# Kernel tuning notes

Hardware: AMD Instinct MI355X
Metric: run time of the kernel (lower is better)

The kernel has to match this reference:

```python
import jax, jax.numpy as jnp
import numpy as np

WS = 8  # window_size

def conv2d(x, w, b, padding=0, dilation=1, groups=1):
    out = jax.lax.conv_general_dilated(
        x, w, window_strides=(1, 1),
        padding=[(padding, padding), (padding, padding)],
        rhs_dilation=(dilation, dilation),
        feature_group_count=groups)
    return out + b[None, :, None, None]

def lrelu(x):
    return jnp.where(x >= 0, x, 0.1 * x)

def ln_cf(x, w, b, eps=1e-6):
    # LayerNorm, channels_first: normalize over channel dim per pixel
    u = x.mean(1, keepdims=True)
    s = ((x - u) ** 2).mean(1, keepdims=True)
    x = (x - u) / jnp.sqrt(s + eps)
    return w[None, :, None, None] * x + b[None, :, None, None]

def window_part(x, ws):
    # b c (h dh) (w dw) -> b (h w) (dh dw c)
    b, c, H, W = x.shape
    h, w = H // ws, W // ws
    x = x.reshape(b, c, h, ws, w, ws).transpose(0, 2, 4, 3, 5, 1)
    return x.reshape(b, h * w, ws * ws * c)

def window_rev(x, ws, H, W, c):
    # b (h w) (dh dw c) -> b c (h dh) (w dw)
    b = x.shape[0]
    h, w = H // ws, W // ws
    x = x.reshape(b, h, w, ws, ws, c).transpose(0, 5, 1, 3, 2, 4)
    return x.reshape(b, c, H, W)

def setup_inputs() -> dict:
    key = jax.random.key(0)
    B, C, H, W = 4, 64, 256, 256
    ws = WS
    E = ws * ws * C  # 4096
    ks = iter(jax.random.split(key, 40))
    def rn(shape, scale=1.0):
        return jax.random.normal(next(ks), shape, jnp.float32) * scale
    z = lambda *s: jnp.zeros(s, jnp.float32)
    d = {}
    d['x'] = rn((B, C, H, W))
    d['Wv'] = rn((C, C, 1, 1), C ** -0.5); d['bv'] = z(C)
    d['Wri'] = rn((C // 4, C, 1, 1), C ** -0.5); d['bri'] = z(C // 4)
    d['Wrc'] = rn((C // 4, C, 1, 1), C ** -0.5); d['brc'] = z(C // 4)
    d['ln_w'] = jnp.ones((C // 4,), jnp.float32); d['ln_b'] = z(C // 4)
    d['Wca'] = rn((C, C // 4, 1, 1), (C // 4) ** -0.5); d['bca'] = z(C)
    d['Wsa'] = rn((1, C // 4, 3, 3), (9 * C // 4) ** -0.5); d['bsa'] = z(1)
    d['Wm1'] = rn((E // 2, E), E ** -0.5); d['bm1'] = z(E // 2)
    d['Wm2'] = rn((E, E // 2), (E // 2) ** -0.5); d['bm2'] = z(E)
    d['Wq'] = rn((C, C), C ** -0.5); d['bq'] = z(C)
    d['Wk'] = rn((C, C), C ** -0.5); d['bk'] = z(C)
    d['Wd1'] = rn((C, 1, 3, 3), 1.0 / 3.0); d['bd1'] = z(C)
    d['Wd2'] = rn((C, 1, 3, 3), 1.0 / 3.0); d['bd2'] = z(C)
    d['Wo'] = rn((C, C, 1, 1), C ** -0.5); d['bo'] = z(C)
    return d

def reference(x, Wv, bv, Wri, bri, Wrc, brc, ln_w, ln_b, Wca, bca, Wsa, bsa,
              Wm1, bm1, Wm2, bm2, Wq, bq, Wk, bk, Wd1, bd1, Wd2, bd2, Wo, bo):
    B, C, H, W = x.shape
    ws = WS
    E = ws * ws * C
    v = conv2d(x, Wv, bv)
    # ---- MaskPre (route) ----
    x1 = lrelu(conv2d(v, Wri, bri))                       # [B,C/4,H,W]
    x_ = lrelu(ln_cf(conv2d(v, Wrc, brc), ln_w, ln_b))    # [B,C/4,H,W]
    ca = jax.nn.sigmoid(conv2d(x_.mean((2, 3), keepdims=True), Wca, bca))  # [B,C,1,1]
    sa = jax.nn.sigmoid(conv2d(x_, Wsa, bsa, padding=1))                   # [B,1,H,W]
    xm = window_part(x1.mean(1, keepdims=True), ws)       # [B,N,ws^2]
    var_x = jnp.var(xm, axis=-1, ddof=1)                  # torch.var is unbiased
    N = var_x.shape[1]
    k_top = N // 2
    _, idx = jax.lax.top_k(-var_x, k_top)                 # k smallest-variance windows
    mask_bin = jnp.ones((B, N), x.dtype).at[jnp.arange(B)[:, None], idx].set(0.0)
    m = jnp.broadcast_to(mask_bin[:, :, None], (B, N, E))
    m = lrelu(m @ Wm1.T + bm1)
    mask = m @ Wm2.T + bm2                                # [B,N,E]
    # ---- windowed attention / skip split ----
    vs = v * sa
    vw = window_part(v, ws)                               # [B,N,ws^2*C]
    vsw = window_part(vs, ws)
    qkw = window_part(jnp.concatenate([x, x], axis=1), ws)  # [B,N,ws^2*2C]
    v1 = vw * mask
    v2 = vsw * (1.0 - mask)
    mask_qk = jnp.concatenate(
        [mask.reshape(B, N, ws * ws, C)] * 2, axis=-1).reshape(B, N, ws * ws * 2 * C)
    qk1 = (qkw * mask_qk).reshape(B, N * ws * ws, 2 * C)
    q1 = (qk1[..., :C] @ Wq.T + bq).reshape(B * N, ws * ws, C)
    k1 = (qk1[..., C:] @ Wk.T + bk).reshape(B * N, ws * ws, C)
    v1r = v1.reshape(B * N, ws * ws, C)
    attn = jax.nn.softmax(q1 @ jnp.swapaxes(k1, -1, -2), axis=-1)  # [BN,ws^2,ws^2]
    f_attn = (attn @ v1r).reshape(B, N, ws * ws * C)
    attn_out = f_attn + v2
    out = window_rev(attn_out, ws, H, W, C)               # [B,C,H,W]
    # ---- spatial conv branch + projections ----
    c1 = conv2d(out, Wd1, bd1, padding=1, groups=C)
    c2 = conv2d(c1, Wd2, bd2, padding=2, dilation=2, groups=C)
    out = jax.nn.gelu(c2, approximate=False) * ca + out
    out = conv2d(out, Wo, bo)
    return out
```

## Files before the change

kernel.cpp:

```cpp
#include <hip/hip_runtime.h>
#include <hip/hip_bf16.h>
#include <math.h>

typedef __attribute__((ext_vector_type(8))) short short8;
typedef __attribute__((ext_vector_type(16))) float f32x16;

__device__ __forceinline__ float lrelu(float x){ return x >= 0.f ? x : 0.1f*x; }
__device__ __forceinline__ float sigmoidf(float x){ return 1.f/(1.f+expf(-x)); }
__device__ __forceinline__ short f2bf(float f){
  __hip_bfloat16 hb = __float2bfloat16(f);
  return *reinterpret_cast<short*>(&hb);
}
__device__ __forceinline__ float bf16f(short s){
  return __uint_as_float(((unsigned)(unsigned short)s)<<16);
}

#define WF(w,part,mt,kt) ((((w)*8 + (part)*4 + (mt)*... 0)
#undef WF
__device__ __forceinline__ int WFofs(int w,int part,int mt,int kt){
  return (((w*2+part)*2+mt)*4+kt)*512;
}

__global__ void k0_combine(const float* __restrict__ Wv, const float* __restrict__ bv,
                           const float* __restrict__ Wri, const float* __restrict__ bri,
                           const float* __restrict__ Wrc, const float* __restrict__ brc,
                           float* __restrict__ WriE, float* __restrict__ briE,
                           float* __restrict__ WrcE, float* __restrict__ brcE){
  int idx = blockIdx.x*256 + threadIdx.x;
  if (idx < 1024){
    int j = idx>>6, c = idx&63;
    float s1=0.f, s2=0.f;
    for (int k=0;k<64;k++){ s1 = fmaf(Wri[j*64+k], Wv[k*64+c], s1); s2 = fmaf(Wrc[j*64+k], Wv[k*64+c], s2); }
    WriE[idx]=s1; WrcE[idx]=s2;
  }
  if (idx < 16){
    float s1=bri[idx], s2=brc[idx];
    for (int k=0;k<64;k++){ s1 = fmaf(Wri[idx*64+k], bv[k], s1); s2 = fmaf(Wrc[idx*64+k], bv[k], s2); }
    briE[idx]=s1; brcE[idx]=s2;
  }
}

__global__ void k_prep(const float* __restrict__ Wq, const float* __restrict__ Wk,
                       const float* __restrict__ Wo, const float* __restrict__ Wv,
                       const float* __restrict__ WriE, const float* __restrict__ WrcE,
                       float* __restrict__ WT, short* __restrict__ WFrag){
  int idx = blockIdx.x*256 + threadIdx.x;
  if (idx < 4096){
    int oc = idx>>6, c = idx&63;
    WT[c*96 + oc] = Wv[idx];
  } else if (idx < 6144){
    int t = idx - 4096;
    int j = (t>>6) & 15, c = t & 63;
    if (t < 1024) WT[c*96 + 64 + j] = WriE[j*64+c];
    else          WT[c*96 + 80 + j] = WrcE[j*64+c];
  }
  if (idx < 3072){
    int w = idx>>10, rem = idx&1023;
    int part = rem>>9, mt = (rem>>8)&1, kt = (rem>>6)&3, lane = rem&63;
    const float* W = (w==0)?Wq:((w==1)?Wk:Wo);
    int j = (mt<<5)|(lane&31);
    int hh = lane>>5;
    short8 frag;
    #pragma unroll
    for (int i=0;i<8;i++){
      int kl = (hh<<2) + (i&3) + ((i>>2)<<3);
      float val = W[j*64 + (kt<<4) + kl];
      short hi = f2bf(val);
      frag[i] = part ? f2bf(val - bf16f(hi)) : hi;
    }
    *(short8*)&WFrag[WFofs(w,part,mt,kt) + (lane<<3)] = frag;
  }
}

__global__ void k_premask1(const float* __restrict__ Wm1, const float* __restrict__ bm1,
                           float* __restrict__ mrow1, float* __restrict__ mrow0){
  __shared__ float red[256];
  int j = blockIdx.x, tid = threadIdx.x;
  const float* row = Wm1 + (size_t)j*4096;
  float s=0.f;
  for (int e=tid;e<4096;e+=256) s += row[e];
  red[tid]=s; __syncthreads();
  for (int o=128;o;o>>=1){ if (tid<o) red[tid]+=red[tid+o]; __syncthreads(); }
  if (tid==0){
    float t = red[0]+bm1[j];
    mrow1[j] = lrelu(t);
    mrow0[j] = lrelu(bm1[j]);
  }
}

__global__ void k_premask2(const float* __restrict__ Wm2, const float* __restrict__ bm2,
                           const float* __restrict__ mrow1, const float* __restrict__ mrow0,
                           float* __restrict__ mask1, float* __restrict__ mask0,
                           float* __restrict__ mask1T, float* __restrict__ mask0T){
  __shared__ float r1[256], r0[256];
  int e = blockIdx.x, tid = threadIdx.x;
  const float* row = Wm2 + (size_t)e*2048;
  float s1=0.f, s0=0.f;
  for (int j=tid;j<2048;j+=256){ float wv=row[j]; s1 = fmaf(wv, mrow1[j], s1); s0 = fmaf(wv, mrow0[j], s0); }
  r1[tid]=s1; r0[tid]=s0; __syncthreads();
  for (int o=128;o;o>>=1){ if (tid<o){ r1[tid]+=r1[tid+o]; r0[tid]+=r0[tid+o]; } __syncthreads(); }
  if (tid==0){
    float m1 = r1[0]+bm2[e], m0 = r0[0]+bm2[e];
    mask1[e]=m1; mask0[e]=m0;
    int p = e>>6, c = e&63;
    mask1T[(c<<6)|p]=m1; mask0T[(c<<6)|p]=m0;
  }
}

__global__ __launch_bounds__(256) void k1_pw(
    const float* __restrict__ x, const float* __restrict__ WT,
    const float* __restrict__ bv,
    const float* __restrict__ briE, const float* __restrict__ brcE,
    const float* __restrict__ ln_w, const float* __restrict__ ln_b,
    float* __restrict__ v, float* __restrict__ x_, float* __restrict__ xm,
    float* __restrict__ bsum){
  __shared__ float wred[4][16];
  int tid = threadIdx.x;
  int b = blockIdx.x >> 8;
  int hw = ((blockIdx.x & 255) << 8) | tid;
  const float* xb = x + (((size_t)b)<<22) + hw;
  float acc[64], r1[16], rc[16];
  #pragma unroll
  for (int oc=0;oc<64;oc++) acc[oc]=0.f;
  #pragma unroll
  for (int j=0;j<16;j++){ r1[j]=0.f; rc[j]=0.f; }
  for (int c=0;c<64;c++){
    float xv = xb[((size_t)c)<<16];
    const float* wrow = WT + c*96;
    #pragma unroll
    for (int oc=0;oc<64;oc++) acc[oc] = fmaf(wrow[oc], xv, acc[oc]);
    #pragma unroll
    for (int j=0;j<16;j++){ r1[j] = fmaf(wrow[64+j], xv, r1[j]); rc[j] = fmaf(wrow[80+j], xv, rc[j]); }
  }
  float* vb = v + (((size_t)b)<<22) + hw;
  #pragma unroll
  for (int oc=0;oc<64;oc++) vb[((size_t)oc)<<16] = acc[oc] + bv[oc];
  float s1=0.f;
  #pragma unroll
  for (int j=0;j<16;j++){ float t = r1[j]+briE[j]; s1 += lrelu(t); }
  xm[(((size_t)b)<<16)+hw] = s1*(1.f/16.f);
  float u=0.f;
  #pragma unroll
  for (int j=0;j<16;j++){ rc[j] += brcE[j]; u += rc[j]; }
  u *= (1.f/16.f);
  float s2=0.f;
  #pragma unroll
  for (int j=0;j<16;j++){ float d = rc[j]-u; s2 += d*d; }
  float inv = 1.0f / sqrtf(s2*(1.f/16.f) + 1e-6f);
  float xs[16];
  #pragma unroll
  for (int j=0;j<16;j++){
    float t = (rc[j]-u)*inv*ln_w[j] + ln_b[j];
    t = lrelu(t);
    xs[j]=t;
    x_[(((size_t)(b*16+j))<<16)+hw] = t;
  }
  int lane = tid & 63, wv_ = tid >> 6;
  #pragma unroll
  for (int j=0;j<16;j++){
    float val = xs[j];
    for (int o=32;o;o>>=1) val += __shfl_down(val, o, 64);
    if (lane==0) wred[wv_][j]=val;
  }
  __syncthreads();
  if (tid<16) bsum[blockIdx.x*16+tid] = wred[0][tid]+wred[1][tid]+wred[2][tid]+wred[3][tid];
}

__global__ __launch_bounds__(256) void k2_sa(const float* __restrict__ x_,
    const float* __restrict__ Wsa, const float* __restrict__ bsa, float* __restrict__ sa){
  int idx = blockIdx.x*256 + threadIdx.x;
  int b = idx>>16; int hw = idx & 65535; int h = hw>>8, wcol = hw & 255;
  float acc = bsa[0];
  for (int ch=0; ch<16; ++ch){
    const float* plane = x_ + (((size_t)(b*16+ch))<<16);
    #pragma unroll
    for (int ky=0;ky<3;ky++){
      int y = h + ky - 1;
      if ((unsigned)y >= 256u) continue;
      #pragma unroll
      for (int kx=0;kx<3;kx++){
        int xx = wcol + kx - 1;
        if ((unsigned)xx >= 256u) continue;
        acc = fmaf(Wsa[ch*9+ky*3+kx], plane[(y<<8)+xx], acc);
      }
    }
  }
  sa[idx] = sigmoidf(acc);
}

__global__ void k3_ca(const float* __restrict__ bsum, const float* __restrict__ Wca,
                      const float* __restrict__ bca, float* __restrict__ ca){
  __shared__ float meanx[4][16];
  int tid = threadIdx.x;
  if (tid < 64){
    int b = tid>>4, j = tid&15;
    float s=0.f;
    for (int blk=0;blk<256;blk++) s += bsum[(b*256+blk)*16 + j];
    meanx[b][j] = s*(1.f/65536.f);
  }
  __syncthreads();
  int b = tid>>6, oc = tid&63;
  float a = bca[oc];
  #pragma unroll
  for (int j=0;j<16;j++) a = fmaf(Wca[oc*16+j], meanx[b][j], a);
  ca[tid] = sigmoidf(a);
}

__global__ void k4a_var(const float* __restrict__ xm, float* __restrict__ var){
  int t = blockIdx.x*256 + threadIdx.x;
  int b = t>>10, n = t&1023, wh = n>>5, ww = n&31;
  const float* base = xm + (((size_t)b)<<16) + (wh<<11) + (ww<<3);
  float s=0.f;
  #pragma unroll
  for (int dh=0;dh<8;dh++){
    #pragma unroll
    for (int dw=0;dw<8;dw++) s += base[(dh<<8)+dw];
  }
  float mean = s*(1.f/64.f);
  float ss=0.f;
  #pragma unroll
  for (int dh=0;dh<8;dh++){
    #pragma unroll
    for (int dw=0;dw<8;dw++){ float d = base[(dh<<8)+dw]-mean; ss += d*d; }
  }
  var[t] = ss*(1.f/63.f);
}

__global__ __launch_bounds__(1024) void k4b_sel(const float* __restrict__ var, float* __restrict__ sel){
  __shared__ float vs[1024];
  int b = blockIdx.x, tid = threadIdx.x;
  float mine = var[b*1024+tid];
  vs[tid]=mine; __syncthreads();
  int rank=0;
  for (int j=0;j<1024;j++){
    float o = vs[j];
    rank += (o < mine) || (o == mine && j < tid);
  }
  sel[b*1024+tid] = (rank >= 512) ? 1.f : 0.f;
}

__global__ __launch_bounds__(256, 3) void k6_attn(
    const float* __restrict__ x, const float* __restrict__ v, const float* __restrict__ sa,
    const float* __restrict__ sel,
    const float* __restrict__ mask1, const float* __restrict__ mask0,
    const float* __restrict__ mask1T, const float* __restrict__ mask0T,
    const short* __restrict__ WFrag,
    const float* __restrict__ bq, const float* __restrict__ bk,
    float* __restrict__ out){
  __shared__ short8 KAlds[2][2][8][64];
  int tid = threadIdx.x;
  int lane = tid & 63, wvi = tid >> 6;
  int wi = wvi >> 1, ht = wvi & 1;
  int l31 = lane & 31, h = lane >> 5;
  int bid = blockIdx.x;
  int blk = ((bid & 7) << 8) | (bid >> 3);
  int wg = (blk << 1) | wi;
  int b = wg >> 10, n = wg & 1023;
  int pix0 = ((n >> 5) << 11) | ((n & 31) << 3);
  bool sel1 = sel[wg] > 0.5f;
  const float* mrow  = sel1 ? mask1  : mask0;
  const float* mrowT = sel1 ? mask1T : mask0T;
  size_t cbase = (((size_t)b) << 22) + pix0;

  int p = (ht<<5) | l31;
  int po = ((p>>3)<<8) | (p&7);
  size_t gp = cbase + po;
  const float* mr = mrow + (p<<6);
  short8 XBh[4], XBl[4];
  #pragma unroll
  for (int kt=0;kt<4;kt++){
    float4 ma = *(const float4*)&mr[(kt<<4)+(h<<2)];
    float4 mb = *(const float4*)&mr[(kt<<4)+(h<<2)+8];
    float xv[8];
    #pragma unroll
    for (int i=0;i<8;i++){
      int c = (kt<<4) + (h<<2) + (i&3) + ((i>>2)<<3);
      xv[i] = x[gp + ((size_t)c<<16)];
    }
    xv[0]*=ma.x; xv[1]*=ma.y; xv[2]*=ma.z; xv[3]*=ma.w;
    xv[4]*=mb.x; xv[5]*=mb.y; xv[6]*=mb.z; xv[7]*=mb.w;
    short8 fh, fl;
    #pragma unroll
    for (int i=0;i<8;i++){
      short hi = f2bf(xv[i]); fh[i]=hi; fl[i]=f2bf(xv[i]-bf16f(hi));
    }
    XBh[kt]=fh; XBl[kt]=fl;
  }

  short8 QBh[4], QBl[4];
  #pragma unroll
  for (int mt=0;mt<2;mt++){
    f32x16 acc;
    #pragma unroll
    for (int r=0;r<16;r++) acc[r]=0.f;
    #pragma unroll
    for (int kt=0;kt<4;kt++){
      short8 WAh = *(const short8*)&WFrag[WFofs(0,0,mt,kt) + (lane<<3)];
      short8 WAl = *(const short8*)&WFrag[WFofs(0,1,mt,kt) + (lane<<3)];
      acc = __builtin_amdgcn_mfma_f32_32x32x16_bf16(WAh, XBh[kt], acc, 0,0,0);
      acc = __builtin_amdgcn_mfma_f32_32x32x16_bf16(WAh, XBl[kt], acc, 0,0,0);
      acc = __builtin_amdgcn_mfma_f32_32x32x16_bf16(WAl, XBh[kt], acc, 0,0,0);
    }
    #pragma unroll
    for (int rr=0;rr<4;rr++){
      float4 b4 = *(const float4*)&bq[(mt<<5)+(rr<<3)+(h<<2)];
      acc[4*rr+0]+=b4.x; acc[4*rr+1]+=b4.y; acc[4*rr+2]+=b4.z; acc[4*rr+3]+=b4.w;
    }
    #pragma unroll
    for (int kk=0;kk<2;kk++){
      short8 fh, fl;
      #pragma unroll
      for (int i=0;i<8;i++){
        float vv = acc[8*kk+i];
        short hi = f2bf(vv); fh[i]=hi; fl[i]=f2bf(vv-bf16f(hi));
      }
      QBh[2*mt+kk]=fh; QBl[2*mt+kk]=fl;
    }
  }

  #pragma unroll
  for (int mt=0;mt<2;mt++){
    f32x16 acc;
    #pragma unroll
    for (int r=0;r<16;r++) acc[r]=0.f;
    #pragma unroll
    for (int kt=0;kt<4;kt++){
      short8 WAh = *(const short8*)&WFrag[WFofs(1,0,mt,kt) + (lane<<3)];
      short8 WAl = *(const short8*)&WFrag[WFofs(1,1,mt,kt) + (lane<<3)];
      acc = __builtin_amdgcn_mfma_f32_32x32x16_bf16(WAh, XBh[kt], acc, 0,0,0);
      acc = __builtin_amdgcn_mfma_f32_32x32x16_bf16(WAh, XBl[kt], acc, 0,0,0);
      acc = __builtin_amdgcn_mfma_f32_32x32x16_bf16(WAl, XBh[kt], acc, 0,0,0);
    }
    #pragma unroll
    for (int rr=0;rr<4;rr++){
      float4 b4 = *(const float4*)&bk[(mt<<5)+(rr<<3)+(h<<2)];
      acc[4*rr+0]+=b4.x; acc[4*rr+1]+=b4.y; acc[4*rr+2]+=b4.z; acc[4*rr+3]+=b4.w;
    }
    #pragma unroll
    for (int kk=0;kk<2;kk++){
      short8 fh, fl;
      #pragma unroll
      for (int i=0;i<8;i++){
        float vv = acc[8*kk+i];
        short hi = f2bf(vv); fh[i]=hi; fl[i]=f2bf(vv-bf16f(hi));
      }
      KAlds[wi][ht][2*mt+kk][lane]   = fh;
      KAlds[wi][ht][4+2*mt+kk][lane] = fl;
    }
  }
  __syncthreads();

  f32x16 ST[2];
  #pragma unroll
  for (int mt=0;mt<2;mt++){
    f32x16 acc;
    #pragma unroll
    for (int r=0;r<16;r++) acc[r]=0.f;
    #pragma unroll
    for (int kt=0;kt<4;kt++){
      short8 kh = KAlds[wi][mt][kt][lane];
      short8 kl = KAlds[wi][mt][4+kt][lane];
      acc = __builtin_amdgcn_mfma_f32_32x32x16_bf16(kh, QBh[kt], acc, 0,0,0);
      acc = __builtin_amdgcn_mfma_f32_32x32x16_bf16(kh, QBl[kt], acc, 0,0,0);
      acc = __builtin_amdgcn_mfma_f32_32x32x16_bf16(kl, QBh[kt], acc, 0,0,0);
    }
    ST[mt] = acc;
  }

  float mx = ST[0][0];
  #pragma unroll
  for (int r=1;r<16;r++) mx = fmaxf(mx, ST[0][r]);
  #pragma unroll
  for (int r=0;r<16;r++) mx = fmaxf(mx, ST[1][r]);
  mx = fmaxf(mx, __shfl_xor(mx, 32));
  float sum = 0.f;
  #pragma unroll
  for (int mt=0;mt<2;mt++)
    #pragma unroll
    for (int r=0;r<16;r++){ float e = expf(ST[mt][r]-mx); ST[mt][r]=e; sum += e; }
  sum += __shfl_xor(sum, 32);
  float inv = 1.f/sum;

  short8 PB[4];
  #pragma unroll
  for (int mt=0;mt<2;mt++)
    #pragma unroll
    for (int kk=0;kk<2;kk++){
      short8 f;
      #pragma unroll
      for (int i=0;i<8;i++) f[i] = f2bf(ST[mt][8*kk+i]*inv);
      PB[2*mt+kk]=f;
    }

  float sav = sa[(((size_t)b)<<16) + pix0 + po];

  #pragma unroll
  for (int mtc=0;mtc<2;mtc++){
    int c0 = (mtc<<5);
    int cl = c0 | l31;
    const float* vp = v + cbase + ((size_t)cl<<16);
    const float* mTr = mrowT + (cl<<6);
    f32x16 acc;
    #pragma unroll
    for (int r=0;r<16;r++) acc[r]=0.f;
    #pragma unroll
    for (int kt=0;kt<4;kt++){
      float4 va  = *(const float4*)&vp[((kt<<1)<<8) + (h<<2)];
      float4 vb2 = *(const float4*)&vp[(((kt<<1)|1)<<8) + (h<<2)];
      float4 ma = *(const float4*)&mTr[(kt<<4)+(h<<2)];
      float4 mb = *(const float4*)&mTr[(kt<<4)+(h<<2)+8];
      short8 f;
      f[0]=f2bf(va.x*ma.x); f[1]=f2bf(va.y*ma.y); f[2]=f2bf(va.z*ma.z); f[3]=f2bf(va.w*ma.w);
      f[4]=f2bf(vb2.x*mb.x); f[5]=f2bf(vb2.y*mb.y); f[6]=f2bf(vb2.z*mb.z); f[7]=f2bf(vb2.w*mb.w);
      acc = __builtin_amdgcn_mfma_f32_32x32x16_bf16(f, PB[kt], acc, 0,0,0);
    }
    #pragma unroll
    for (int rr=0;rr<4;rr++){
      float4 m4 = *(const float4*)&mr[c0+(rr<<3)+(h<<2)];
      #pragma unroll
      for (int t=0;t<4;t++){
        int c = c0 + (rr<<3) + (h<<2) + t;
        size_t g = cbase + ((size_t)c<<16) + po;
        float vv = v[g];
        float mm = (t==0)?m4.x:(t==1)?m4.y:(t==2)?m4.z:m4.w;
        out[g] = acc[4*rr+t] + sav*vv*(1.f-mm);
      }
    }
  }
}

__global__ __launch_bounds__(256) void k7_fused(const float* __restrict__ in,
    const float* __restrict__ Wd1, const float* __restrict__ bd1,
    const float* __restrict__ Wd2, const float* __restrict__ bd2,
    const float* __restrict__ ca, float* __restrict__ dwout){
  __shared__ float IN[22*23];
  __shared__ float C1[20*21];
  int blk = blockIdx.x;
  int tx = blk & 15, ty = (blk>>4) & 15, ch = (blk>>8) & 63, b = blk>>14;
  int x0 = tx<<4, y0 = ty<<4;
  const float* plane = in + (((size_t)(b*64+ch))<<16);
  int tid = threadIdx.x;
  for (int e = tid; e < 484; e += 256){
    int r = e/22, cc = e - r*22;
    int y = y0 + r - 3, xx = x0 + cc - 3;
    float vv = 0.f;
    if ((unsigned)y < 256u && (unsigned)xx < 256u) vv = plane[(y<<8)+xx];
    IN[r*23+cc] = vv;
  }
  __syncthreads();
  float w1[9], w2[9];
  #pragma unroll
  for (int t=0;t<9;t++){ w1[t]=Wd1[ch*9+t]; w2[t]=Wd2[ch*9+t]; }
  float b1 = bd1[ch];
  for (int e = tid; e < 400; e += 256){
    int r = e/20, cc = e - r*20;
    int yc1 = y0 + r - 2, xc1 = x0 + cc - 2;
    float acc = 0.f;
    if ((unsigned)yc1 < 256u && (unsigned)xc1 < 256u){
      acc = b1;
      #pragma unroll
      for (int ky=0;ky<3;ky++)
        #pragma unroll
        for (int kx=0;kx<3;kx++)
          acc = fmaf(w1[ky*3+kx], IN[(r+ky)*23 + cc+kx], acc);
    }
    C1[r*21+cc] = acc;
  }
  __syncthreads();
  int px = tid & 15, py = tid >> 4;
  float acc = bd2[ch];
  #pragma unroll
  for (int ky=0;ky<3;ky++)
    #pragma unroll
    for (int kx=0;kx<3;kx++)
      acc = fmaf(w2[ky*3+kx], C1[(py+2*ky)*21 + px+2*kx], acc);
  float g = 0.5f*acc*(1.f + erff(acc*0.70710678118654752f));
  float resid = IN[(py+3)*23 + px+3];
  size_t o = (((size_t)(b*64+ch))<<16) + ((size_t)((y0+py)<<8)) + x0+px;
  dwout[o] = fmaf(g, ca[b*64+ch], resid);
}

__global__ __launch_bounds__(256, 3) void k7c_proj(const float* __restrict__ in,
    const short* __restrict__ WFrag, const float* __restrict__ bo,
    float* __restrict__ out){
  int tid = threadIdx.x;
  int lane = tid & 63, wvi = tid >> 6;
  int l31 = lane & 31, h = lane >> 5;
  int blk = blockIdx.x;
  int b = blk >> 8;
  int hw0 = ((blk & 255) << 8) | (wvi << 6);
  size_t base = ((size_t)b) << 22;
  #pragma unroll
  for (int nt=0;nt<2;nt++){
    int px = hw0 | (nt<<5) | l31;
    short8 XH[4], XL[4];
    #pragma unroll
    for (int kt=0;kt<4;kt++){
      float xv[8];
      #pragma unroll
      for (int i=0;i<8;i++){
        int c = (kt<<4) + (h<<2) + (i&3) + ((i>>2)<<3);
        xv[i] = in[base + ((size_t)c<<16) + px];
      }
      short8 fh, fl;
      #pragma unroll
      for (int i=0;i<8;i++){
        short hi = f2bf(xv[i]); fh[i]=hi; fl[i]=f2bf(xv[i]-bf16f(hi));
      }
      XH[kt]=fh; XL[kt]=fl;
    }
    #pragma unroll
    for (int mt=0;mt<2;mt++){
      f32x16 acc;
      #pragma unroll
      for (int r=0;r<16;r++) acc[r]=0.f;
      #pragma unroll
      for (int kt=0;kt<4;kt++){
        short8 WAh = *(const short8*)&WFrag[WFofs(2,0,mt,kt) + (lane<<3)];
        short8 WAl = *(const short8*)&WFrag[WFofs(2,1,mt,kt) + (lane<<3)];
        acc = __builtin_amdgcn_mfma_f32_32x32x16_bf16(WAh, XH[kt], acc, 0,0,0);
        acc = __builtin_amdgcn_mfma_f32_32x32x16_bf16(WAh, XL[kt], acc, 0,0,0);
        acc = __builtin_amdgcn_mfma_f32_32x32x16_bf16(WAl, XH[kt], acc, 0,0,0);
      }
      #pragma unroll
      for (int rr=0;rr<4;rr++){
        float4 b4 = *(const float4*)&bo[(mt<<5)+(rr<<3)+(h<<2)];
        #pragma unroll
        for (int t=0;t<4;t++){
          int oc = (mt<<5) + (rr<<3) + (h<<2) + t;
          float bb = (t==0)?b4.x:(t==1)?b4.y:(t==2)?b4.z:b4.w;
          out[base + ((size_t)oc<<16) + px] = acc[4*rr+t] + bb;
        }
      }
    }
  }
}

extern "C" void kernel_launch(void* const* d_in, const int* in_sizes, int n_in,
                              void* d_out, int out_size, void* d_ws, size_t ws_size,
                              hipStream_t stream) {
  const float* x    = (const float*)d_in[0];
  const float* Wv   = (const float*)d_in[1];
  const float* bv   = (const float*)d_in[2];
  const float* Wri  = (const float*)d_in[3];
  const float* bri  = (const float*)d_in[4];
  const float* Wrc  = (const float*)d_in[5];
  const float* brc  = (const float*)d_in[6];
  const float* ln_w = (const float*)d_in[7];
  const float* ln_b = (const float*)d_in[8];
  const float* Wca  = (const float*)d_in[9];
  const float* bca  = (const float*)d_in[10];
  const float* Wsa  = (const float*)d_in[11];
  const float* bsa  = (const float*)d_in[12];
  const float* Wm1  = (const float*)d_in[13];
  const float* bm1  = (const float*)d_in[14];
  const float* Wm2  = (const float*)d_in[15];
  const float* bm2  = (const float*)d_in[16];
  const float* Wq   = (const float*)d_in[17];
  const float* bq   = (const float*)d_in[18];
  const float* Wk   = (const float*)d_in[19];
  const float* bk   = (const float*)d_in[20];
  const float* Wd1  = (const float*)d_in[21];
  const float* bd1  = (const float*)d_in[22];
  const float* Wd2  = (const float*)d_in[23];
  const float* bd2  = (const float*)d_in[24];
  const float* Wo   = (const float*)d_in[25];
  const float* bo   = (const float*)d_in[26];
  float* out = (float*)d_out;

  float* ws = (float*)d_ws;
  float* v_buf   = ws;
  float* out_buf = v_buf + 16777216;
  float* x_buf   = out_buf + 16777216;
  float* xm_buf  = x_buf + 4194304;
  float* sa_buf  = xm_buf + 262144;
  float* bsum    = sa_buf + 262144;
  float* ca_buf  = bsum + 16384;
  float* var_buf = ca_buf + 256;
  float* sel_buf = var_buf + 4096;
  float* mrow1   = sel_buf + 4096;
  float* mrow0   = mrow1 + 2048;
  float* mask1   = mrow0 + 2048;
  float* mask0   = mask1 + 4096;
  float* mask1T  = mask0 + 4096;
  float* mask0T  = mask1T + 4096;
  float* WT      = mask0T + 4096;
  float* WriE    = WT + 6144;
  float* WrcE    = WriE + 1024;
  float* briE    = WrcE + 1024;
  float* brcE    = briE + 16;
  short* WFrag   = (short*)(brcE + 16);
  float* dw_buf  = v_buf;

  k0_combine<<<4,256,0,stream>>>(Wv,bv,Wri,bri,Wrc,brc,WriE,briE,WrcE,brcE);
  k_prep<<<24,256,0,stream>>>(Wq,Wk,Wo,Wv,WriE,WrcE,WT,WFrag);
  k_premask1<<<2048,256,0,stream>>>(Wm1,bm1,mrow1,mrow0);
  k_premask2<<<4096,256,0,stream>>>(Wm2,bm2,mrow1,mrow0,mask1,mask0,mask1T,mask0T);
  k1_pw<<<1024,256,0,stream>>>(x,WT,bv,briE,brcE,ln_w,ln_b,v_buf,x_buf,xm_buf,bsum);
  k2_sa<<<1024,256,0,stream>>>(x_buf,Wsa,bsa,sa_buf);
  k3_ca<<<1,256,0,stream>>>(bsum,Wca,bca,ca_buf);
  k4a_var<<<16,256,0,stream>>>(xm_buf,var_buf);
  k4b_sel<<<4,1024,0,stream>>>(var_buf,sel_buf);
  k6_attn<<<2048,256,0,stream>>>(x,v_buf,sa_buf,sel_buf,mask1,mask0,mask1T,mask0T,WFrag,bq,bk,out_buf);
  k7_fused<<<65536,256,0,stream>>>(out_buf,Wd1,bd1,Wd2,bd2,ca_buf,dw_buf);
  k7c_proj<<<1024,256,0,stream>>>(dw_buf,WFrag,bo,out);
}
```

Measured before the change: 393.0 us.

## Move pointwise projection to split-bf16 MFMA and enlarge depthwise conv tiles

The first pointwise kernel (v, ri and rc projections) now uses 32x32x16 bf16 MFMA with a hi/lo split (three products per step) instead of per-thread scalar FMAs. Its weights are packed into fragment form in the prep kernel, and the channel reductions are done with cross-lane shuffles. The fused depthwise conv kernel now uses 32x32 tiles instead of 16x16, which lowers halo overhead and block count, and k6_attn's occupancy hint goes from 3 to 5. The split-bf16 scheme keeps near-fp32 accuracy, but the larger conv tiles use more LDS and the occupancy change may force register spills.

```diff
diff --git a/kernel.cpp b/kernel.cpp
--- a/kernel.cpp
+++ b/kernel.cpp
@@ -15,8 +15,6 @@
   return __uint_as_float(((unsigned)(unsigned short)s)<<16);
 }
 
-#define WF(w,part,mt,kt) ((((w)*8 + (part)*4 + (mt)*... 0)
-#undef WF
 __device__ __forceinline__ int WFofs(int w,int part,int mt,int kt){
   return (((w*2+part)*2+mt)*4+kt)*512;
 }
@@ -43,28 +41,28 @@
 __global__ void k_prep(const float* __restrict__ Wq, const float* __restrict__ Wk,
                        const float* __restrict__ Wo, const float* __restrict__ Wv,
                        const float* __restrict__ WriE, const float* __restrict__ WrcE,
-                       float* __restrict__ WT, short* __restrict__ WFrag){
+                       short* __restrict__ WFrag){
   int idx = blockIdx.x*256 + threadIdx.x;
-  if (idx < 4096){
-    int oc = idx>>6, c = idx&63;
-    WT[c*96 + oc] = Wv[idx];
-  } else if (idx < 6144){
-    int t = idx - 4096;
-    int j = (t>>6) & 15, c = t & 63;
-    if (t < 1024) WT[c*96 + 64 + j] = WriE[j*64+c];
-    else          WT[c*96 + 80 + j] = WrcE[j*64+c];
-  }
-  if (idx < 3072){
+  if (idx < 6144){
     int w = idx>>10, rem = idx&1023;
     int part = rem>>9, mt = (rem>>8)&1, kt = (rem>>6)&3, lane = rem&63;
-    const float* W = (w==0)?Wq:((w==1)?Wk:Wo);
-    int j = (mt<<5)|(lane&31);
     int hh = lane>>5;
     short8 frag;
     #pragma unroll
     for (int i=0;i<8;i++){
       int kl = (hh<<2) + (i&3) + ((i>>2)<<3);
-      float val = W[j*64 + (kt<<4) + kl];
+      int kfull = (kt<<4) + kl;
+      float val = 0.f;
+      if (w < 3){
+        const float* W = (w==0)?Wq:((w==1)?Wk:Wo);
+        int j = (mt<<5)|(lane&31);
+        val = W[j*64 + kfull];
+      } else if (mt == 0){
+        int j = lane&31;
+        if (w==3)      val = Wv[j*64 + kfull];
+        else if (w==4) val = Wv[(32+j)*64 + kfull];
+        else           val = (j<16) ? WriE[j*64 + kfull] : WrcE[(j-16)*64 + kfull];
+      }
       short hi = f2bf(val);
       frag[i] = part ? f2bf(val - bf16f(hi)) : hi;
     }
@@ -107,63 +105,101 @@
   }
 }
 
-__global__ __launch_bounds__(256) void k1_pw(
-    const float* __restrict__ x, const float* __restrict__ WT,
+__global__ __launch_bounds__(256, 4) void k1_pw(
+    const float* __restrict__ x, const short* __restrict__ WFrag,
     const float* __restrict__ bv,
     const float* __restrict__ briE, const float* __restrict__ brcE,
     const float* __restrict__ ln_w, const float* __restrict__ ln_b,
     float* __restrict__ v, float* __restrict__ x_, float* __restrict__ xm,
     float* __restrict__ bsum){
   __shared__ float wred[4][16];
-  int tid = threadIdx.x;
-  int b = blockIdx.x >> 8;
-  int hw = ((blockIdx.x & 255) << 8) | tid;
-  const float* xb = x + (((size_t)b)<<22) + hw;
-  float acc[64], r1[16], rc[16];
-  #pragma unroll
-  for (int oc=0;oc<64;oc++) acc[oc]=0.f;
-  #pragma unroll
-  for (int j=0;j<16;j++){ r1[j]=0.f; rc[j]=0.f; }
-  for (int c=0;c<64;c++){
-    float xv = xb[((size_t)c)<<16];
-    const float* wrow = WT + c*96;
-    #pragma unroll
-    for (int oc=0;oc<64;oc++) acc[oc] = fmaf(wrow[oc], xv, acc[oc]);
-    #pragma unroll
-    for (int j=0;j<16;j++){ r1[j] = fmaf(wrow[64+j], xv, r1[j]); rc[j] = fmaf(wrow[80+j], xv, rc[j]); }
-  }
-  float* vb = v + (((size_t)b)<<22) + hw;
-  #pragma unroll
-  for (int oc=0;oc<64;oc++) vb[((size_t)oc)<<16] = acc[oc] + bv[oc];
-  float s1=0.f;
-  #pragma unroll
-  for (int j=0;j<16;j++){ float t = r1[j]+briE[j]; s1 += lrelu(t); }
-  xm[(((size_t)b)<<16)+hw] = s1*(1.f/16.f);
-  float u=0.f;
-  #pragma unroll
-  for (int j=0;j<16;j++){ rc[j] += brcE[j]; u += rc[j]; }
+  int tid = threadIdx.x, lane = tid&63, wvi = tid>>6, l31 = lane&31, h = lane>>5;
+  int blk = blockIdx.x;
+  int b = blk>>9;
+  int hw = ((blk&511)<<7) | (wvi<<5) | l31;
+  size_t xb = (((size_t)b)<<22) + hw;
+  short8 XH[4], XL[4];
+  #pragma unroll
+  for (int kt=0;kt<4;kt++){
+    float xv[8];
+    #pragma unroll
+    for (int i=0;i<8;i++){
+      int c = (kt<<4) + (h<<2) + (i&3) + ((i>>2)<<3);
+      xv[i] = x[xb + ((size_t)c<<16)];
+    }
+    short8 fh, fl;
+    #pragma unroll
+    for (int i=0;i<8;i++){ short hi=f2bf(xv[i]); fh[i]=hi; fl[i]=f2bf(xv[i]-bf16f(hi)); }
+    XH[kt]=fh; XL[kt]=fl;
+  }
+  f32x16 T[3];
+  #pragma unroll
+  for (int t3=0;t3<3;t3++){
+    f32x16 acc;
+    #pragma unroll
+    for (int r=0;r<16;r++) acc[r]=0.f;
+    #pragma unroll
+    for (int kt=0;kt<4;kt++){
+      short8 WAh = *(const short8*)&WFrag[WFofs(3+t3,0,0,kt) + (lane<<3)];
+      short8 WAl = *(const short8*)&WFrag[WFofs(3+t3,1,0,kt) + (lane<<3)];
+      acc = __builtin_amdgcn_mfma_f32_32x32x16_bf16(WAh, XH[kt], acc, 0,0,0);
+      acc = __builtin_amdgcn_mfma_f32_32x32x16_bf16(WAh, XL[kt], acc, 0,0,0);
+      acc = __builtin_amdgcn_mfma_f32_32x32x16_bf16(WAl, XH[kt], acc, 0,0,0);
+    }
+    T[t3]=acc;
+  }
+  #pragma unroll
+  for (int r=0;r<16;r++){
+    int c0 = (r&3) + ((r>>2)<<3) + (h<<2);
+    v[xb + ((size_t)c0<<16)]      = T[0][r] + bv[c0];
+    v[xb + ((size_t)(c0+32)<<16)] = T[1][r] + bv[c0+32];
+  }
+  float s1 = 0.f;
+  #pragma unroll
+  for (int r=0;r<8;r++){
+    int j = (r&3) + ((r>>2)<<3) + (h<<2);
+    s1 += lrelu(T[2][r] + briE[j]);
+  }
+  s1 += __shfl_xor(s1, 32);
+  xm[(((size_t)b)<<16) + hw] = s1*(1.f/16.f);
+  float vals[8], u = 0.f;
+  #pragma unroll
+  for (int r=0;r<8;r++){
+    int j = (r&3) + ((r>>2)<<3) + (h<<2);
+    float t = T[2][8+r] + brcE[j];
+    vals[r]=t; u += t;
+  }
+  u += __shfl_xor(u, 32);
   u *= (1.f/16.f);
-  float s2=0.f;
-  #pragma unroll
-  for (int j=0;j<16;j++){ float d = rc[j]-u; s2 += d*d; }
+  float s2 = 0.f;
+  #pragma unroll
+  for (int r=0;r<8;r++){ float d = vals[r]-u; s2 += d*d; }
+  s2 += __shfl_xor(s2, 32);
   float inv = 1.0f / sqrtf(s2*(1.f/16.f) + 1e-6f);
-  float xs[16];
-  #pragma unroll
-  for (int j=0;j<16;j++){
-    float t = (rc[j]-u)*inv*ln_w[j] + ln_b[j];
-    t = lrelu(t);
-    xs[j]=t;
-    x_[(((size_t)(b*16+j))<<16)+hw] = t;
-  }
-  int lane = tid & 63, wv_ = tid >> 6;
-  #pragma unroll
-  for (int j=0;j<16;j++){
-    float val = xs[j];
-    for (int o=32;o;o>>=1) val += __shfl_down(val, o, 64);
-    if (lane==0) wred[wv_][j]=val;
+  float bs[8];
+  #pragma unroll
+  for (int r=0;r<8;r++){
+    int j = (r&3) + ((r>>2)<<3) + (h<<2);
+    float t = lrelu((vals[r]-u)*inv*ln_w[j] + ln_b[j]);
+    x_[(((size_t)(b*16+j))<<16) + hw] = t;
+    bs[r]=t;
+  }
+  #pragma unroll
+  for (int r=0;r<8;r++){
+    float val = bs[r];
+    val += __shfl_xor(val,1); val += __shfl_xor(val,2); val += __shfl_xor(val,4);
+    val += __shfl_xor(val,8); val += __shfl_xor(val,16);
+    bs[r]=val;
+  }
+  if (l31==0){
+    #pragma unroll
+    for (int r=0;r<8;r++){
+      int j = (r&3) + ((r>>2)<<3) + (h<<2);
+      wred[wvi][j] = bs[r];
+    }
   }
   __syncthreads();
-  if (tid<16) bsum[blockIdx.x*16+tid] = wred[0][tid]+wred[1][tid]+wred[2][tid]+wred[3][tid];
+  if (tid<16) bsum[blk*16+tid] = wred[0][tid]+wred[1][tid]+wred[2][tid]+wred[3][tid];
 }
 
 __global__ __launch_bounds__(256) void k2_sa(const float* __restrict__ x_,
@@ -195,7 +231,7 @@
   if (tid < 64){
     int b = tid>>4, j = tid&15;
     float s=0.f;
-    for (int blk=0;blk<256;blk++) s += bsum[(b*256+blk)*16 + j];
+    for (int blk=0;blk<512;blk++) s += bsum[(b*512+blk)*16 + j];
     meanx[b][j] = s*(1.f/65536.f);
   }
   __syncthreads();
@@ -239,7 +275,7 @@
   sel[b*1024+tid] = (rank >= 512) ? 1.f : 0.f;
 }
 
-__global__ __launch_bounds__(256, 3) void k6_attn(
+__global__ __launch_bounds__(256, 5) void k6_attn(
     const float* __restrict__ x, const float* __restrict__ v, const float* __restrict__ sa,
     const float* __restrict__ sel,
     const float* __restrict__ mask1, const float* __restrict__ mask0,
@@ -433,27 +469,29 @@
     const float* __restrict__ Wd1, const float* __restrict__ bd1,
     const float* __restrict__ Wd2, const float* __restrict__ bd2,
     const float* __restrict__ ca, float* __restrict__ dwout){
-  __shared__ float IN[22*23];
-  __shared__ float C1[20*21];
+  __shared__ float IN[38*39];
+  __shared__ float C1[36*37];
   int blk = blockIdx.x;
-  int tx = blk & 15, ty = (blk>>4) & 15, ch = (blk>>8) & 63, b = blk>>14;
-  int x0 = tx<<4, y0 = ty<<4;
+  int tile = blk & 63;
+  int tx = tile & 7, ty = tile >> 3;
+  int ch = (blk>>6) & 63, b = blk>>12;
+  int x0 = tx<<5, y0 = ty<<5;
   const float* plane = in + (((size_t)(b*64+ch))<<16);
   int tid = threadIdx.x;
-  for (int e = tid; e < 484; e += 256){
-    int r = e/22, cc = e - r*22;
+  for (int e = tid; e < 1444; e += 256){
+    int r = e/38, cc = e - r*38;
     int y = y0 + r - 3, xx = x0 + cc - 3;
     float vv = 0.f;
     if ((unsigned)y < 256u && (unsigned)xx < 256u) vv = plane[(y<<8)+xx];
-    IN[r*23+cc] = vv;
+    IN[r*39+cc] = vv;
   }
   __syncthreads();
   float w1[9], w2[9];
   #pragma unroll
   for (int t=0;t<9;t++){ w1[t]=Wd1[ch*9+t]; w2[t]=Wd2[ch*9+t]; }
   float b1 = bd1[ch];
-  for (int e = tid; e < 400; e += 256){
-    int r = e/20, cc = e - r*20;
+  for (int e = tid; e < 1296; e += 256){
+    int r = e/36, cc = e - r*36;
     int yc1 = y0 + r - 2, xc1 = x0 + cc - 2;
     float acc = 0.f;
     if ((unsigned)yc1 < 256u && (unsigned)xc1 < 256u){
@@ -462,22 +500,28 @@
       for (int ky=0;ky<3;ky++)
         #pragma unroll
         for (int kx=0;kx<3;kx++)
-          acc = fmaf(w1[ky*3+kx], IN[(r+ky)*23 + cc+kx], acc);
-    }
-    C1[r*21+cc] = acc;
+          acc = fmaf(w1[ky*3+kx], IN[(r+ky)*39 + cc+kx], acc);
+    }
+    C1[r*37+cc] = acc;
   }
   __syncthreads();
-  int px = tid & 15, py = tid >> 4;
-  float acc = bd2[ch];
-  #pragma unroll
-  for (int ky=0;ky<3;ky++)
-    #pragma unroll
-    for (int kx=0;kx<3;kx++)
-      acc = fmaf(w2[ky*3+kx], C1[(py+2*ky)*21 + px+2*kx], acc);
-  float g = 0.5f*acc*(1.f + erff(acc*0.70710678118654752f));
-  float resid = IN[(py+3)*23 + px+3];
-  size_t o = (((size_t)(b*64+ch))<<16) + ((size_t)((y0+py)<<8)) + x0+px;
-  dwout[o] = fmaf(g, ca[b*64+ch], resid);
+  int px = tid & 31, py0 = tid >> 5;
+  float cav = ca[b*64+ch];
+  float b2 = bd2[ch];
+  #pragma unroll
+  for (int q=0;q<4;q++){
+    int py = py0 + (q<<3);
+    float acc = b2;
+    #pragma unroll
+    for (int ky=0;ky<3;ky++)
+      #pragma unroll
+      for (int kx=0;kx<3;kx++)
+        acc = fmaf(w2[ky*3+kx], C1[(py+2*ky)*37 + px+2*kx], acc);
+    float g = 0.5f*acc*(1.f + erff(acc*0.70710678118654752f));
+    float resid = IN[(py+3)*39 + px+3];
+    size_t o = (((size_t)(b*64+ch))<<16) + ((size_t)((y0+py)<<8)) + x0+px;
+    dwout[o] = fmaf(g, cav, resid);
+  }
 }
 
 __global__ __launch_bounds__(256, 3) void k7c_proj(const float* __restrict__ in,
@@ -575,7 +619,7 @@
   float* xm_buf  = x_buf + 4194304;
   float* sa_buf  = xm_buf + 262144;
   float* bsum    = sa_buf + 262144;
-  float* ca_buf  = bsum + 16384;
+  float* ca_buf  = bsum + 32768;
   float* var_buf = ca_buf + 256;
   float* sel_buf = var_buf + 4096;
   float* mrow1   = sel_buf + 4096;
@@ -584,8 +628,7 @@
   float* mask0   = mask1 + 4096;
   float* mask1T  = mask0 + 4096;
   float* mask0T  = mask1T + 4096;
-  float* WT      = mask0T + 4096;
-  float* WriE    = WT + 6144;
+  float* WriE    = mask0T + 4096;
   float* WrcE    = WriE + 1024;
   float* briE    = WrcE + 1024;
   float* brcE    = briE + 16;
@@ -593,15 +636,15 @@
   float* dw_buf  = v_buf;
 
   k0_combine<<<4,256,0,stream>>>(Wv,bv,Wri,bri,Wrc,brc,WriE,briE,WrcE,brcE);
-  k_prep<<<24,256,0,stream>>>(Wq,Wk,Wo,Wv,WriE,WrcE,WT,WFrag);
+  k_prep<<<24,256,0,stream>>>(Wq,Wk,Wo,Wv,WriE,WrcE,WFrag);
   k_premask1<<<2048,256,0,stream>>>(Wm1,bm1,mrow1,mrow0);
   k_premask2<<<4096,256,0,stream>>>(Wm2,bm2,mrow1,mrow0,mask1,mask0,mask1T,mask0T);
-  k1_pw<<<1024,256,0,stream>>>(x,WT,bv,briE,brcE,ln_w,ln_b,v_buf,x_buf,xm_buf,bsum);
+  k1_pw<<<2048,256,0,stream>>>(x,WFrag,bv,briE,brcE,ln_w,ln_b,v_buf,x_buf,xm_buf,bsum);
   k2_sa<<<1024,256,0,stream>>>(x_buf,Wsa,bsa,sa_buf);
   k3_ca<<<1,256,0,stream>>>(bsum,Wca,bca,ca_buf);
   k4a_var<<<16,256,0,stream>>>(xm_buf,var_buf);
   k4b_sel<<<4,1024,0,stream>>>(var_buf,sel_buf);
   k6_attn<<<2048,256,0,stream>>>(x,v_buf,sa_buf,sel_buf,mask1,mask0,mask1T,mask0T,WFrag,bq,bk,out_buf);
-  k7_fused<<<65536,256,0,stream>>>(out_buf,Wd1,bd1,Wd2,bd2,ca_buf,dw_buf);
+  k7_fused<<<16384,256,0,stream>>>(out_buf,Wd1,bd1,Wd2,bd2,ca_buf,dw_buf);
   k7c_proj<<<1024,256,0,stream>>>(dw_buf,WFrag,bo,out);
 }
```

New measurement: 399.2 us. Within noise of the previous version (+1.6%).
